# Kernel tuning notes

Hardware: AMD Instinct MI355X
Metric: run time of the kernel (lower is better)

The kernel has to match this reference:

```python
import jax, jax.numpy as jnp
import numpy as np

EMBED = 1024
HEADS = 16
HEAD_DIM = EMBED // HEADS
SCALE = HEAD_DIM ** -0.5


def setup_inputs() -> dict:
    key = jax.random.key(0)
    ks = jax.random.split(key, 9)
    B, N = 2, 2048
    std = EMBED ** -0.5
    return {
        "query": jax.random.normal(ks[0], (B, N, EMBED), jnp.float32),
        "key": jax.random.normal(ks[1], (B, N, EMBED), jnp.float32),
        "value": jax.random.normal(ks[2], (B, N, EMBED), jnp.float32),
        # torch nn.Linear weights are [out, in]; y = x @ W.T + b
        "Wq": jax.random.normal(ks[3], (EMBED, EMBED), jnp.float32) * std,
        "bq": jax.random.normal(ks[4], (EMBED,), jnp.float32) * 0.01,
        "Wk": jax.random.normal(ks[5], (EMBED, EMBED), jnp.float32) * std,
        "bk": jax.random.normal(ks[6], (EMBED,), jnp.float32) * 0.01,
        "Wv": jax.random.normal(ks[7], (EMBED, EMBED), jnp.float32) * std,
        "bv": jax.random.normal(ks[8], (EMBED,), jnp.float32) * 0.01,
    }


def reference(query, key, value, Wq, bq, Wk, bk, Wv, bv):
    B, NQ, _ = query.shape
    NK = key.shape[1]
    q = query @ Wq.T + bq  # [B, NQ, E]
    k = key @ Wk.T + bk    # [B, NK, E]
    v = value @ Wv.T + bv  # [B, NK, E]
    # split heads -> [B, H, N, Dh]
    q = q.reshape(B, NQ, HEADS, HEAD_DIM).transpose(0, 2, 1, 3)
    k = k.reshape(B, NK, HEADS, HEAD_DIM).transpose(0, 2, 1, 3)
    v = v.reshape(B, NK, HEADS, HEAD_DIM).transpose(0, 2, 1, 3)
    attn = jnp.einsum("bhqd,bhkd->bhqk", q, k) * SCALE  # [B, H, NQ, NK]
    attn = jax.nn.softmax(attn, axis=-1)
    out = jnp.einsum("bhqk,bhkd->bhqd", attn, v)  # [B, H, NQ, Dh]
    out = out.transpose(0, 2, 1, 3).reshape(B, NQ, EMBED)
    # o_proj is Identity (odim == embed_dim, o_proj=False); dropout is 0 (eval)
    return out
```

## Files before the change

### kernel.cpp

```cpp
#include <hip/hip_runtime.h>

#define EMB 1024
#define NSEQ 2048
#define NBATCH 2
#define NHEAD 16
#define DHEAD 64
#define QSCALE 0.18033688011112042f

typedef float f32x4 __attribute__((ext_vector_type(4)));
typedef short s16x8 __attribute__((ext_vector_type(8)));
typedef short s16x4 __attribute__((ext_vector_type(4)));

typedef __attribute__((address_space(3))) short lds_short;
typedef __attribute__((address_space(1))) const short glb_short;

__device__ __forceinline__ void gl_lds16(const short* g, short* l) {
    __builtin_amdgcn_global_load_lds((glb_short*)g, (lds_short*)l, 16, 0, 0);
}

__device__ __forceinline__ short bf16r(float f) {
    unsigned u = __float_as_uint(f);
    u += 0x7fffu + ((u >> 16) & 1u);
    return (short)(u >> 16);
}

__device__ __forceinline__ unsigned pkbf(float a, float b) {
#if defined(__has_builtin) && __has_builtin(__builtin_amdgcn_cvt_pk_bf16_f32)
    auto r = __builtin_amdgcn_cvt_pk_bf16_f32(a, b);
    unsigned u;
    __builtin_memcpy(&u, &r, 4);
    return u;
#else
    return ((unsigned)bf16r(a) & 0xffffu) | ((unsigned)bf16r(b) << 16);
#endif
}

__device__ __forceinline__ float fexp2(float x) {
#if defined(__has_builtin) && __has_builtin(__builtin_amdgcn_exp2f)
    return __builtin_amdgcn_exp2f(x);
#else
    return exp2f(x);
#endif
}

__global__ __launch_bounds__(256) void cvt6_kernel(
    const float* __restrict__ s0, const float* __restrict__ s1, const float* __restrict__ s2,
    const float* __restrict__ s3, const float* __restrict__ s4, const float* __restrict__ s5,
    short* __restrict__ d0, short* __restrict__ d1, short* __restrict__ d2,
    short* __restrict__ d3, short* __restrict__ d4, short* __restrict__ d5,
    int n0, int n1, int n2, int n3, int n4, int n5)
{
    const int seg = blockIdx.y;
    const float* s = (seg == 0) ? s0 : (seg == 1) ? s1 : (seg == 2) ? s2
                   : (seg == 3) ? s3 : (seg == 4) ? s4 : s5;
    short* d = (seg == 0) ? d0 : (seg == 1) ? d1 : (seg == 2) ? d2
             : (seg == 3) ? d3 : (seg == 4) ? d4 : d5;
    const int n = (seg == 0) ? n0 : (seg == 1) ? n1 : (seg == 2) ? n2
                : (seg == 3) ? n3 : (seg == 4) ? n4 : n5;

    const int i = (blockIdx.x * 256 + threadIdx.x) * 8;
    if (i >= n) return;
    float4 a = *(const float4*)(s + i);
    float4 b = *(const float4*)(s + i + 4);
    uint4 u = { pkbf(a.x, a.y), pkbf(a.z, a.w), pkbf(b.x, b.y), pkbf(b.z, b.w) };
    *(uint4*)(d + i) = u;
}

__global__ __launch_bounds__(256, 3) void proj2_kernel(
    const short* __restrict__ Xq, const short* __restrict__ Xk, const short* __restrict__ Xv,
    const short* __restrict__ Wq, const short* __restrict__ Wk, const short* __restrict__ Wv,
    const float* __restrict__ bq, const float* __restrict__ bk, const float* __restrict__ bv,
    short* __restrict__ Oq, short* __restrict__ Ok, short* __restrict__ Ov)
{
    const int z = blockIdx.z;
    const short* X    = (z == 0) ? Xq : (z == 1) ? Xk : Xv;
    const short* W    = (z == 0) ? Wq : (z == 1) ? Wk : Wv;
    const float* bias = (z == 0) ? bq : (z == 1) ? bk : bv;
    short* Out        = (z == 0) ? Oq : (z == 1) ? Ok : Ov;
    const float osc   = (z == 0) ? QSCALE : 1.0f;

    const int n0 = blockIdx.x * 128;
    const int m0 = blockIdx.y * 128;

    __shared__ __align__(16) short As[128 * 64];
    __shared__ __align__(16) short Bs[128 * 64];

    const int t    = threadIdx.x;
    const int lane = t & 63;
    const int wave = t >> 6;
    const int r    = lane & 15;
    const int quad = lane >> 4;
    const int wm   = (wave >> 1) * 64;
    const int wn   = (wave & 1) * 64;

    const int p0    = wave * 256 + lane;
    const int row0  = p0 >> 3;
    const int lc0   = (p0 & 7) ^ (row0 & 7);
    const short* gA = X + (size_t)(m0 + row0) * EMB + lc0 * 8;
    const short* gB = W + (size_t)(n0 + row0) * EMB + lc0 * 8;
    short* lA = As + p0 * 8;
    short* lB = Bs + p0 * 8;

    f32x4 acc[4][4];
#pragma unroll
    for (int i = 0; i < 4; ++i)
#pragma unroll
        for (int j = 0; j < 4; ++j)
#pragma unroll
            for (int v = 0; v < 4; ++v) acc[i][j][v] = 0.f;

    for (int k0 = 0; k0 < EMB; k0 += 64) {
#pragma unroll
        for (int i = 0; i < 4; ++i) {
            gl_lds16(gA + k0 + (size_t)8 * i * EMB, lA + i * 512);
            gl_lds16(gB + k0 + (size_t)8 * i * EMB, lB + i * 512);
        }
        __syncthreads();

#pragma unroll
        for (int ks = 0; ks < 2; ++ks) {
            const int fc = ((ks * 4 + quad) ^ (r & 7)) * 8;
            s16x8 af[4], bf[4];
#pragma unroll
            for (int i = 0; i < 4; ++i) af[i] = *(const s16x8*)&As[(wm + i * 16 + r) * 64 + fc];
#pragma unroll
            for (int j = 0; j < 4; ++j) bf[j] = *(const s16x8*)&Bs[(wn + j * 16 + r) * 64 + fc];
#pragma unroll
            for (int i = 0; i < 4; ++i)
#pragma unroll
                for (int j = 0; j < 4; ++j)
                    acc[i][j] = __builtin_amdgcn_mfma_f32_16x16x32_bf16(af[i], bf[j], acc[i][j], 0, 0, 0);
        }
        __syncthreads();
    }

    if (z != 2) {
#pragma unroll
        for (int j = 0; j < 4; ++j) {
            const int gn = n0 + wn + j * 16 + r;
            const float bb = bias[gn];
#pragma unroll
            for (int i = 0; i < 4; ++i)
#pragma unroll
                for (int reg = 0; reg < 4; ++reg) {
                    const int gm = m0 + wm + i * 16 + quad * 4 + reg;
                    Out[(size_t)gm * EMB + gn] = bf16r((acc[i][j][reg] + bb) * osc);
                }
        }
    } else {
#pragma unroll
        for (int j = 0; j < 4; ++j) {
            const int gn = n0 + wn + j * 16 + r;
            const float bb = bias[gn];
            const int hh = gn >> 6;
            const int dd = gn & 63;
#pragma unroll
            for (int i = 0; i < 4; ++i) {
                const int gm = m0 + wm + i * 16 + quad * 4;
                const int bi = gm >> 11;
                const int nn = gm & 2047;
                s16x4 pk;
#pragma unroll
                for (int reg = 0; reg < 4; ++reg) pk[reg] = bf16r(acc[i][j][reg] + bb);
                *(s16x4*)(Out + ((size_t)(bi * NHEAD + hh) * DHEAD + dd) * NSEQ + nn) = pk;
            }
        }
    }
}

__global__ __launch_bounds__(256) void proj_kernel(
    const float* __restrict__ Xq, const float* __restrict__ Xk, const float* __restrict__ Xv,
    const float* __restrict__ Wq, const float* __restrict__ Wk, const float* __restrict__ Wv,
    const float* __restrict__ bq, const float* __restrict__ bk, const float* __restrict__ bv,
    short* __restrict__ Oq, short* __restrict__ Ok, short* __restrict__ Ov)
{
    const int z = blockIdx.z;
    const float* X    = (z == 0) ? Xq : (z == 1) ? Xk : Xv;
    const float* W    = (z == 0) ? Wq : (z == 1) ? Wk : Wv;
    const float* bias = (z == 0) ? bq : (z == 1) ? bk : bv;
    short* Out        = (z == 0) ? Oq : (z == 1) ? Ok : Ov;
    const float osc   = (z == 0) ? QSCALE : 1.0f;

    const int n0 = blockIdx.x * 128;
    const int m0 = blockIdx.y * 128;

    __shared__ __align__(16) short As[128][40];
    __shared__ __align__(16) short Bs[128][40];

    const int t    = threadIdx.x;
    const int lane = t & 63;
    const int wave = t >> 6;
    const int r    = lane & 15;
    const int quad = lane >> 4;
    const int wm   = (wave >> 1) * 64;
    const int wn   = (wave & 1) * 64;

    const int srow = t >> 1;
    const int scol = (t & 1) << 4;

    f32x4 acc[4][4];
#pragma unroll
    for (int i = 0; i < 4; ++i)
#pragma unroll
        for (int j = 0; j < 4; ++j)
#pragma unroll
            for (int v = 0; v < 4; ++v) acc[i][j][v] = 0.f;

    for (int k0 = 0; k0 < EMB; k0 += 32) {
        const float4* xp = (const float4*)(X + (size_t)(m0 + srow) * EMB + k0 + scol);
        const float4* wp = (const float4*)(W + (size_t)(n0 + srow) * EMB + k0 + scol);
        float4 x0 = xp[0], x1 = xp[1], x2 = xp[2], x3 = xp[3];
        float4 w0 = wp[0], w1 = wp[1], w2 = wp[2], w3 = wp[3];
        uint4 a0 = { pkbf(x0.x, x0.y), pkbf(x0.z, x0.w), pkbf(x1.x, x1.y), pkbf(x1.z, x1.w) };
        uint4 a1 = { pkbf(x2.x, x2.y), pkbf(x2.z, x2.w), pkbf(x3.x, x3.y), pkbf(x3.z, x3.w) };
        uint4 b0 = { pkbf(w0.x, w0.y), pkbf(w0.z, w0.w), pkbf(w1.x, w1.y), pkbf(w1.z, w1.w) };
        uint4 b1 = { pkbf(w2.x, w2.y), pkbf(w2.z, w2.w), pkbf(w3.x, w3.y), pkbf(w3.z, w3.w) };
        *(uint4*)&As[srow][scol]     = a0;
        *(uint4*)&As[srow][scol + 8] = a1;
        *(uint4*)&Bs[srow][scol]     = b0;
        *(uint4*)&Bs[srow][scol + 8] = b1;
        __syncthreads();

        s16x8 af[4], bf[4];
#pragma unroll
        for (int i = 0; i < 4; ++i) af[i] = *(const s16x8*)&As[wm + i * 16 + r][quad * 8];
#pragma unroll
        for (int j = 0; j < 4; ++j) bf[j] = *(const s16x8*)&Bs[wn + j * 16 + r][quad * 8];
#pragma unroll
        for (int i = 0; i < 4; ++i)
#pragma unroll
            for (int j = 0; j < 4; ++j)
                acc[i][j] = __builtin_amdgcn_mfma_f32_16x16x32_bf16(af[i], bf[j], acc[i][j], 0, 0, 0);
        __syncthreads();
    }

#pragma unroll
    for (int j = 0; j < 4; ++j) {
        const int gn = n0 + wn + j * 16 + r;
        const float bb = bias[gn];
#pragma unroll
        for (int i = 0; i < 4; ++i)
#pragma unroll
            for (int reg = 0; reg < 4; ++reg) {
                const int gm = m0 + wm + i * 16 + quad * 4 + reg;
                Out[(size_t)gm * EMB + gn] = bf16r((acc[i][j][reg] + bb) * osc);
            }
    }
}

__global__ __launch_bounds__(256) void vtrans_kernel(
    const short* __restrict__ Vp, short* __restrict__ VT)
{
    const int n0 = blockIdx.x * 64;
    const int h  = blockIdx.y;
    const int b  = blockIdx.z;
    __shared__ __align__(16) short L[64][72];

    const int t  = threadIdx.x;
    const int rr = t >> 2;
    const int cc = (t & 3) * 16;

    const short* src = Vp + (size_t)(b * NSEQ + n0 + rr) * EMB + h * DHEAD + cc;
    s16x8 a = *(const s16x8*)src;
    s16x8 c = *(const s16x8*)(src + 8);
    *(s16x8*)&L[rr][cc]     = a;
    *(s16x8*)&L[rr][cc + 8] = c;
    __syncthreads();

    const int d  = t >> 2;
    const int c4 = (t & 3) * 16;
    short vals[16];
#pragma unroll
    for (int i = 0; i < 16; ++i) vals[i] = L[c4 + i][d];
    short* dst = VT + ((size_t)(b * NHEAD + h) * DHEAD + d) * NSEQ + n0 + c4;
    *(s16x8*)dst       = *(s16x8*)&vals[0];
    *(s16x8*)(dst + 8) = *(s16x8*)&vals[8];
}

__global__ __launch_bounds__(256, 2) void attn12_kernel(
    const short* __restrict__ Qp, const short* __restrict__ Kp,
    const short* __restrict__ VT, float* __restrict__ Out)
{
    const int qblk = blockIdx.x * 128;
    const int h    = blockIdx.y;
    const int b    = blockIdx.z;

    __shared__ __align__(16) char smem[65536];
    short* S    = (short*)smem;
    float* fbuf = (float*)smem;

    const int t    = threadIdx.x;
    const int lane = t & 63;
    const int w    = t >> 6;
    const int r    = lane & 15;
    const int quad = lane >> 4;
    const int r7   = r & 7;

    const size_t rowbase = (size_t)b * NSEQ;
    const int    colbase = h * DHEAD;
    const size_t bh64    = (size_t)(b * NHEAD + h) * DHEAD;

    s16x8 qf[2][2];
#pragma unroll
    for (int qs = 0; qs < 2; ++qs)
#pragma unroll
        for (int ks = 0; ks < 2; ++ks)
            qf[qs][ks] = *(const s16x8*)(Qp + (rowbase + qblk + w * 32 + qs * 16 + r) * EMB
                                          + colbase + ks * 32 + quad * 8);

    f32x4 accO[2][4];
#pragma unroll
    for (int qs = 0; qs < 2; ++qs)
#pragma unroll
        for (int dt = 0; dt < 4; ++dt)
#pragma unroll
            for (int v = 0; v < 4; ++v) accO[qs][dt][v] = 0.f;
    float lsum[2] = {0.f, 0.f};
    const f32x4 zf = {0.f, 0.f, 0.f, 0.f};

    const int krow0 = t >> 3;
    const int kgc   = ((t & 7) ^ (krow0 & 7)) * 8;
    const int vrow0 = t >> 4;
    const int vgc   = ((t & 15) ^ (vrow0 & 7)) * 8;
    const short* gKp = Kp + (rowbase + krow0) * EMB + colbase + kgc;
    const short* gVp = VT + (bh64 + vrow0) * NSEQ + vgc;

    {
        short* SK = S;
        short* SV = S + 8192;
#pragma unroll
        for (int i = 0; i < 4; ++i) {
            gl_lds16(gKp + (size_t)i * 32 * EMB, SK + (i * 256 + t) * 8);
            gl_lds16(gVp + (size_t)i * 16 * NSEQ, SV + (i * 256 + t) * 8);
        }
        gKp += (size_t)128 * EMB;
        gVp += 128;
    }
    __syncthreads();

    const int kofs = (quad ^ r7) * 8;
    int vofs[4];
    {
        const int x4  = r7 & 4;
        const int qr3 = ((quad >> 1) ^ r7) & 3;
#pragma unroll
        for (int s = 0; s < 4; ++s)
            vofs[s] = ((((s << 2) ^ x4) | qr3) * 8) + (quad & 1) * 4;
    }

#pragma unroll 2
    for (int it = 0; it < 16; ++it) {
        const int cur = it & 1;

        if (it + 1 < 16) {
            short* SKn = S + (cur ^ 1) * 16384;
            short* SVn = SKn + 8192;
#pragma unroll
            for (int i = 0; i < 4; ++i) {
                gl_lds16(gKp + (size_t)i * 32 * EMB, SKn + (i * 256 + t) * 8);
                gl_lds16(gVp + (size_t)i * 16 * NSEQ, SVn + (i * 256 + t) * 8);
            }
            gKp += (size_t)128 * EMB;
            gVp += 128;
        }

        const short* Ks = S + cur * 16384;
        const short* Vs = Ks + 8192;

        s16x8 pf[2][4];
#pragma unroll
        for (int s = 0; s < 4; ++s) {
            const short* kb = Ks + (s * 32 + r) * 64;
            const s16x8 kf00 = *(const s16x8*)(kb + kofs);
            const s16x8 kf01 = *(const s16x8*)(kb + (kofs ^ 32));
            const s16x8 kf10 = *(const s16x8*)(kb + 1024 + kofs);
            const s16x8 kf11 = *(const s16x8*)(kb + 1024 + (kofs ^ 32));
#pragma unroll
            for (int qs = 0; qs < 2; ++qs) {
                __builtin_amdgcn_s_setprio(1);
                f32x4 s0 = __builtin_amdgcn_mfma_f32_16x16x32_bf16(
                    kf01, qf[qs][1], __builtin_amdgcn_mfma_f32_16x16x32_bf16(kf00, qf[qs][0], zf, 0, 0, 0), 0, 0, 0);
                f32x4 s1 = __builtin_amdgcn_mfma_f32_16x16x32_bf16(
                    kf11, qf[qs][1], __builtin_amdgcn_mfma_f32_16x16x32_bf16(kf10, qf[qs][0], zf, 0, 0, 0), 0, 0, 0);
                __builtin_amdgcn_s_setprio(0);
                float p0[4], p1[4];
#pragma unroll
                for (int reg = 0; reg < 4; ++reg) {
                    p0[reg] = fexp2(s0[reg]);
                    p1[reg] = fexp2(s1[reg]);
                    lsum[qs] += p0[reg] + p1[reg];
                }
                uint4 uu = { pkbf(p0[0], p0[1]), pkbf(p0[2], p0[3]),
                             pkbf(p1[0], p1[1]), pkbf(p1[2], p1[3]) };
                __builtin_memcpy(&pf[qs][s], &uu, 16);
            }
        }

#pragma unroll
        for (int dt = 0; dt < 4; ++dt) {
            const short* vb = Vs + (dt * 16 + r) * 128;
            s16x8 vfl[4];
#pragma unroll
            for (int s = 0; s < 4; ++s) {
                s16x4 lo = *(const s16x4*)(vb + vofs[s]);
                s16x4 hi = *(const s16x4*)(vb + (vofs[s] ^ 16));
                vfl[s] = __builtin_shufflevector(lo, hi, 0, 1, 2, 3, 4, 5, 6, 7);
            }
            __builtin_amdgcn_s_setprio(1);
#pragma unroll
            for (int qs = 0; qs < 2; ++qs)
#pragma unroll
                for (int s = 0; s < 4; ++s)
                    accO[qs][dt] = __builtin_amdgcn_mfma_f32_16x16x32_bf16(vfl[s], pf[qs][s], accO[qs][dt], 0, 0, 0);
            __builtin_amdgcn_s_setprio(0);
        }

        __syncthreads();
    }

    float rl[2];
#pragma unroll
    for (int qs = 0; qs < 2; ++qs) {
        float s = lsum[qs];
        s += __shfl_xor(s, 16);
        s += __shfl_xor(s, 32);
        rl[qs] = 1.f / s;
    }

#pragma unroll
    for (int qs = 0; qs < 2; ++qs) {
        __syncthreads();
#pragma unroll
        for (int dt = 0; dt < 4; ++dt)
#pragma unroll
            for (int reg = 0; reg < 4; ++reg)
                fbuf[(w * 16 + r) * 68 + dt * 16 + quad * 4 + reg] = accO[qs][dt][reg] * rl[qs];
        __syncthreads();
        const int qi   = t >> 2;
        const int c    = (t & 3) * 16;
        const int wsrc = qi >> 4;
        const int rsrc = qi & 15;
        const float4* fp = (const float4*)&fbuf[(wsrc * 16 + rsrc) * 68 + c];
        float4 o0 = fp[0], o1 = fp[1], o2 = fp[2], o3 = fp[3];
        float* op = Out + (rowbase + qblk + wsrc * 32 + qs * 16 + rsrc) * EMB + colbase + c;
        ((float4*)op)[0] = o0;
        ((float4*)op)[1] = o1;
        ((float4*)op)[2] = o2;
        ((float4*)op)[3] = o3;
    }
}

__global__ __launch_bounds__(256) void attn_fb_kernel(
    const short* __restrict__ Qp, const short* __restrict__ Kp,
    const short* __restrict__ Vp, float* __restrict__ Out)
{
    const int qt = blockIdx.x;
    const int h  = blockIdx.y;
    const int b  = blockIdx.z;

    __shared__ __align__(16) short Ks[64][72];
    __shared__ __align__(16) short VsT[64][72];
    __shared__ __align__(16) short Ps[4][16][72];

    const int t    = threadIdx.x;
    const int lane = t & 63;
    const int w    = t >> 6;
    const int r    = lane & 15;
    const int quad = lane >> 4;

    const size_t rowbase = (size_t)b * NSEQ;
    const int colbase    = h * DHEAD;

    const short* Qr = Qp + (rowbase + qt * 64 + w * 16 + r) * EMB + colbase;
    const s16x8 qf0 = *(const s16x8*)(Qr + quad * 8);
    const s16x8 qf1 = *(const s16x8*)(Qr + 32 + quad * 8);

    float mrow[4], lrow[4];
    f32x4 accO[4];
#pragma unroll
    for (int i = 0; i < 4; ++i) {
        mrow[i] = -INFINITY;
        lrow[i] = 0.f;
#pragma unroll
        for (int v = 0; v < 4; ++v) accO[i][v] = 0.f;
    }

    const int srow = t >> 2;
    const int scol = (t & 3) << 4;

    for (int kt = 0; kt < 32; ++kt) {
        const short* Krow = Kp + (rowbase + kt * 64 + srow) * EMB + colbase + scol;
        const short* Vrow = Vp + (rowbase + kt * 64 + srow) * EMB + colbase + scol;
        s16x8 kv0 = *(const s16x8*)Krow;
        s16x8 kv1 = *(const s16x8*)(Krow + 8);
        s16x8 vv0 = *(const s16x8*)Vrow;
        s16x8 vv1 = *(const s16x8*)(Vrow + 8);
        *(s16x8*)&Ks[srow][scol]     = kv0;
        *(s16x8*)&Ks[srow][scol + 8] = kv1;
#pragma unroll
        for (int i = 0; i < 8; ++i) {
            VsT[scol + i][srow]     = vv0[i];
            VsT[scol + 8 + i][srow] = vv1[i];
        }
        __syncthreads();

        f32x4 sacc[4];
#pragma unroll
        for (int j = 0; j < 4; ++j) {
#pragma unroll
            for (int v = 0; v < 4; ++v) sacc[j][v] = 0.f;
            s16x8 kf0 = *(const s16x8*)&Ks[j * 16 + r][quad * 8];
            s16x8 kf1 = *(const s16x8*)&Ks[j * 16 + r][32 + quad * 8];
            sacc[j] = __builtin_amdgcn_mfma_f32_16x16x32_bf16(qf0, kf0, sacc[j], 0, 0, 0);
            sacc[j] = __builtin_amdgcn_mfma_f32_16x16x32_bf16(qf1, kf1, sacc[j], 0, 0, 0);
        }

        float rmax[4];
#pragma unroll
        for (int reg = 0; reg < 4; ++reg) rmax[reg] = -INFINITY;
#pragma unroll
        for (int j = 0; j < 4; ++j)
#pragma unroll
            for (int reg = 0; reg < 4; ++reg)
                rmax[reg] = fmaxf(rmax[reg], sacc[j][reg]);
#pragma unroll
        for (int reg = 0; reg < 4; ++reg) {
#pragma unroll
            for (int mask = 1; mask <= 8; mask <<= 1)
                rmax[reg] = fmaxf(rmax[reg], __shfl_xor(rmax[reg], mask, 64));
        }

        float alpha[4], rsum[4];
#pragma unroll
        for (int reg = 0; reg < 4; ++reg) {
            float mnew = fmaxf(mrow[reg], rmax[reg]);
            alpha[reg] = fexp2(mrow[reg] - mnew);
            mrow[reg]  = mnew;
            rsum[reg]  = 0.f;
        }

#pragma unroll
        for (int j = 0; j < 4; ++j)
#pragma unroll
            for (int reg = 0; reg < 4; ++reg) {
                float p = fexp2(sacc[j][reg] - mrow[reg]);
                rsum[reg] += p;
                Ps[w][quad * 4 + reg][j * 16 + r] = bf16r(p);
            }
#pragma unroll
        for (int reg = 0; reg < 4; ++reg) {
#pragma unroll
            for (int mask = 1; mask <= 8; mask <<= 1)
                rsum[reg] += __shfl_xor(rsum[reg], mask, 64);
            lrow[reg] = lrow[reg] * alpha[reg] + rsum[reg];
        }
#pragma unroll
        for (int j = 0; j < 4; ++j)
#pragma unroll
            for (int reg = 0; reg < 4; ++reg) accO[j][reg] *= alpha[reg];

#pragma unroll
        for (int s = 0; s < 2; ++s) {
            s16x8 pfr = *(const s16x8*)&Ps[w][r][s * 32 + quad * 8];
#pragma unroll
            for (int j = 0; j < 4; ++j) {
                s16x8 vfr = *(const s16x8*)&VsT[j * 16 + r][s * 32 + quad * 8];
                accO[j] = __builtin_amdgcn_mfma_f32_16x16x32_bf16(pfr, vfr, accO[j], 0, 0, 0);
            }
        }
        __syncthreads();
    }

#pragma unroll
    for (int j = 0; j < 4; ++j)
#pragma unroll
        for (int reg = 0; reg < 4; ++reg) {
            const int qrow = qt * 64 + w * 16 + quad * 4 + reg;
            Out[(rowbase + qrow) * EMB + colbase + j * 16 + r] = accO[j][reg] / lrow[reg];
        }
}

extern "C" void kernel_launch(void* const* d_in, const int* in_sizes, int n_in,
                              void* d_out, int out_size, void* d_ws, size_t ws_size,
                              hipStream_t stream) {
    const float* query = (const float*)d_in[0];
    const float* key   = (const float*)d_in[1];
    const float* value = (const float*)d_in[2];
    const float* Wq    = (const float*)d_in[3];
    const float* bq    = (const float*)d_in[4];
    const float* Wk    = (const float*)d_in[5];
    const float* bk    = (const float*)d_in[6];
    const float* Wv    = (const float*)d_in[7];
    const float* bv    = (const float*)d_in[8];
    float* out = (float*)d_out;

    const size_t XBUF = (size_t)NBATCH * NSEQ * EMB;
    const size_t WBUF = (size_t)EMB * EMB;

    short* Qb  = (short*)d_ws;
    short* Kb  = Qb + XBUF;
    short* Vb  = Kb + XBUF;
    short* VTb = Vb + XBUF;
    short* Xqb = VTb + XBUF;
    short* Xkb = Xqb + XBUF;
    short* Xvb = Xkb + XBUF;
    short* Wqb = Xvb + XBUF;
    short* Wkb = Wqb + WBUF;
    short* Wvb = Wkb + WBUF;

    const size_t need_full = (7 * XBUF + 3 * WBUF) * sizeof(short);
    const size_t need_attn = 4 * XBUF * sizeof(short);

    if (ws_size >= need_full) {
        cvt6_kernel<<<dim3(2048, 6), 256, 0, stream>>>(
            query, key, value, Wq, Wk, Wv,
            Xqb, Xkb, Xvb, Wqb, Wkb, Wvb,
            (int)XBUF, (int)XBUF, (int)XBUF, (int)WBUF, (int)WBUF, (int)WBUF);
        proj2_kernel<<<dim3(EMB / 128, (NBATCH * NSEQ) / 128, 3), 256, 0, stream>>>(
            Xqb, Xkb, Xvb, Wqb, Wkb, Wvb, bq, bk, bv, Qb, Kb, VTb);
        attn12_kernel<<<dim3(NSEQ / 128, NHEAD, NBATCH), 256, 0, stream>>>(
            Qb, Kb, VTb, out);
    } else if (ws_size >= need_attn) {
        proj_kernel<<<dim3(EMB / 128, (NBATCH * NSEQ) / 128, 3), 256, 0, stream>>>(
            query, key, value, Wq, Wk, Wv, bq, bk, bv, Qb, Kb, Vb);
        vtrans_kernel<<<dim3(NSEQ / 64, NHEAD, NBATCH), 256, 0, stream>>>(Vb, VTb);
        attn12_kernel<<<dim3(NSEQ / 128, NHEAD, NBATCH), 256, 0, stream>>>(
            Qb, Kb, VTb, out);
    } else {
        proj_kernel<<<dim3(EMB / 128, (NBATCH * NSEQ) / 128, 3), 256, 0, stream>>>(
            query, key, value, Wq, Wk, Wv, bq, bk, bv, Qb, Kb, Vb);
        attn_fb_kernel<<<dim3(NSEQ / 64, NHEAD, NBATCH), 256, 0, stream>>>(Qb, Kb, Vb, out);
    }
}
```

Baseline: 199.6 us.

## Single-buffer attention LDS, compute row sums via MFMA, interleave PV per key slice

```diff
diff --git a/kernel.cpp b/kernel.cpp
--- a/kernel.cpp
+++ b/kernel.cpp
@@ -277,7 +277,7 @@
     *(s16x8*)(dst + 8) = *(s16x8*)&vals[8];
 }
 
-__global__ __launch_bounds__(256, 2) void attn12_kernel(
+__global__ __launch_bounds__(256, 3) void attn13_kernel(
     const short* __restrict__ Qp, const short* __restrict__ Kp,
     const short* __restrict__ VT, float* __restrict__ Out)
 {
@@ -285,8 +285,9 @@
     const int h    = blockIdx.y;
     const int b    = blockIdx.z;
 
-    __shared__ __align__(16) char smem[65536];
-    short* S    = (short*)smem;
+    __shared__ __align__(16) char smem[32768];
+    short* Ks   = (short*)smem;
+    short* Vs   = (short*)smem + 128 * 64;
     float* fbuf = (float*)smem;
 
     const int t    = threadIdx.x;
@@ -309,14 +310,20 @@
                                           + colbase + ks * 32 + quad * 8);
 
     f32x4 accO[2][4];
-#pragma unroll
-    for (int qs = 0; qs < 2; ++qs)
+    f32x4 lacc[2];
+#pragma unroll
+    for (int qs = 0; qs < 2; ++qs) {
+#pragma unroll
+        for (int v = 0; v < 4; ++v) lacc[qs][v] = 0.f;
 #pragma unroll
         for (int dt = 0; dt < 4; ++dt)
 #pragma unroll
             for (int v = 0; v < 4; ++v) accO[qs][dt][v] = 0.f;
-    float lsum[2] = {0.f, 0.f};
+    }
     const f32x4 zf = {0.f, 0.f, 0.f, 0.f};
+    const short one_bf = (short)0x3F80;
+    const s16x8 ones = { one_bf, one_bf, one_bf, one_bf,
+                         one_bf, one_bf, one_bf, one_bf };
 
     const int krow0 = t >> 3;
     const int kgc   = ((t & 7) ^ (krow0 & 7)) * 8;
@@ -325,19 +332,6 @@
     const short* gKp = Kp + (rowbase + krow0) * EMB + colbase + kgc;
     const short* gVp = VT + (bh64 + vrow0) * NSEQ + vgc;
 
-    {
-        short* SK = S;
-        short* SV = S + 8192;
-#pragma unroll
-        for (int i = 0; i < 4; ++i) {
-            gl_lds16(gKp + (size_t)i * 32 * EMB, SK + (i * 256 + t) * 8);
-            gl_lds16(gVp + (size_t)i * 16 * NSEQ, SV + (i * 256 + t) * 8);
-        }
-        gKp += (size_t)128 * EMB;
-        gVp += 128;
-    }
-    __syncthreads();
-
     const int kofs = (quad ^ r7) * 8;
     int vofs[4];
     {
@@ -348,26 +342,16 @@
             vofs[s] = ((((s << 2) ^ x4) | qr3) * 8) + (quad & 1) * 4;
     }
 
-#pragma unroll 2
     for (int it = 0; it < 16; ++it) {
-        const int cur = it & 1;
-
-        if (it + 1 < 16) {
-            short* SKn = S + (cur ^ 1) * 16384;
-            short* SVn = SKn + 8192;
-#pragma unroll
-            for (int i = 0; i < 4; ++i) {
-                gl_lds16(gKp + (size_t)i * 32 * EMB, SKn + (i * 256 + t) * 8);
-                gl_lds16(gVp + (size_t)i * 16 * NSEQ, SVn + (i * 256 + t) * 8);
-            }
-            gKp += (size_t)128 * EMB;
-            gVp += 128;
-        }
-
-        const short* Ks = S + cur * 16384;
-        const short* Vs = Ks + 8192;
-
-        s16x8 pf[2][4];
+#pragma unroll
+        for (int i = 0; i < 4; ++i) {
+            gl_lds16(gKp + (size_t)i * 32 * EMB, Ks + (i * 256 + t) * 8);
+            gl_lds16(gVp + (size_t)i * 16 * NSEQ, Vs + (i * 256 + t) * 8);
+        }
+        gKp += (size_t)128 * EMB;
+        gVp += 128;
+        __syncthreads();
+
 #pragma unroll
         for (int s = 0; s < 4; ++s) {
             const short* kb = Ks + (s * 32 + r) * 64;
@@ -375,6 +359,7 @@
             const s16x8 kf01 = *(const s16x8*)(kb + (kofs ^ 32));
             const s16x8 kf10 = *(const s16x8*)(kb + 1024 + kofs);
             const s16x8 kf11 = *(const s16x8*)(kb + 1024 + (kofs ^ 32));
+            s16x8 pf_s[2];
 #pragma unroll
             for (int qs = 0; qs < 2; ++qs) {
                 __builtin_amdgcn_s_setprio(1);
@@ -383,49 +368,32 @@
                 f32x4 s1 = __builtin_amdgcn_mfma_f32_16x16x32_bf16(
                     kf11, qf[qs][1], __builtin_amdgcn_mfma_f32_16x16x32_bf16(kf10, qf[qs][0], zf, 0, 0, 0), 0, 0, 0);
                 __builtin_amdgcn_s_setprio(0);
-                float p0[4], p1[4];
-#pragma unroll
-                for (int reg = 0; reg < 4; ++reg) {
-                    p0[reg] = fexp2(s0[reg]);
-                    p1[reg] = fexp2(s1[reg]);
-                    lsum[qs] += p0[reg] + p1[reg];
-                }
-                uint4 uu = { pkbf(p0[0], p0[1]), pkbf(p0[2], p0[3]),
-                             pkbf(p1[0], p1[1]), pkbf(p1[2], p1[3]) };
-                __builtin_memcpy(&pf[qs][s], &uu, 16);
+                const float e0 = fexp2(s0[0]), e1 = fexp2(s0[1]);
+                const float e2 = fexp2(s0[2]), e3 = fexp2(s0[3]);
+                const float e4 = fexp2(s1[0]), e5 = fexp2(s1[1]);
+                const float e6 = fexp2(s1[2]), e7 = fexp2(s1[3]);
+                uint4 uu = { pkbf(e0, e1), pkbf(e2, e3), pkbf(e4, e5), pkbf(e6, e7) };
+                __builtin_memcpy(&pf_s[qs], &uu, 16);
+                lacc[qs] = __builtin_amdgcn_mfma_f32_16x16x32_bf16(ones, pf_s[qs], lacc[qs], 0, 0, 0);
             }
-        }
-
-#pragma unroll
-        for (int dt = 0; dt < 4; ++dt) {
-            const short* vb = Vs + (dt * 16 + r) * 128;
-            s16x8 vfl[4];
-#pragma unroll
-            for (int s = 0; s < 4; ++s) {
+#pragma unroll
+            for (int dt = 0; dt < 4; ++dt) {
+                const short* vb = Vs + (dt * 16 + r) * 128;
                 s16x4 lo = *(const s16x4*)(vb + vofs[s]);
                 s16x4 hi = *(const s16x4*)(vb + (vofs[s] ^ 16));
-                vfl[s] = __builtin_shufflevector(lo, hi, 0, 1, 2, 3, 4, 5, 6, 7);
+                s16x8 vfl = __builtin_shufflevector(lo, hi, 0, 1, 2, 3, 4, 5, 6, 7);
+                __builtin_amdgcn_s_setprio(1);
+                accO[0][dt] = __builtin_amdgcn_mfma_f32_16x16x32_bf16(vfl, pf_s[0], accO[0][dt], 0, 0, 0);
+                accO[1][dt] = __builtin_amdgcn_mfma_f32_16x16x32_bf16(vfl, pf_s[1], accO[1][dt], 0, 0, 0);
+                __builtin_amdgcn_s_setprio(0);
             }
-            __builtin_amdgcn_s_setprio(1);
-#pragma unroll
-            for (int qs = 0; qs < 2; ++qs)
-#pragma unroll
-                for (int s = 0; s < 4; ++s)
-                    accO[qs][dt] = __builtin_amdgcn_mfma_f32_16x16x32_bf16(vfl[s], pf[qs][s], accO[qs][dt], 0, 0, 0);
-            __builtin_amdgcn_s_setprio(0);
-        }
-
+        }
         __syncthreads();
     }
 
     float rl[2];
 #pragma unroll
-    for (int qs = 0; qs < 2; ++qs) {
-        float s = lsum[qs];
-        s += __shfl_xor(s, 16);
-        s += __shfl_xor(s, 32);
-        rl[qs] = 1.f / s;
-    }
+    for (int qs = 0; qs < 2; ++qs) rl[qs] = 1.f / lacc[qs][0];
 
 #pragma unroll
     for (int qs = 0; qs < 2; ++qs) {
@@ -618,13 +586,13 @@
             (int)XBUF, (int)XBUF, (int)XBUF, (int)WBUF, (int)WBUF, (int)WBUF);
         proj2_kernel<<<dim3(EMB / 128, (NBATCH * NSEQ) / 128, 3), 256, 0, stream>>>(
             Xqb, Xkb, Xvb, Wqb, Wkb, Wvb, bq, bk, bv, Qb, Kb, VTb);
-        attn12_kernel<<<dim3(NSEQ / 128, NHEAD, NBATCH), 256, 0, stream>>>(
+        attn13_kernel<<<dim3(NSEQ / 128, NHEAD, NBATCH), 256, 0, stream>>>(
             Qb, Kb, VTb, out);
     } else if (ws_size >= need_attn) {
         proj_kernel<<<dim3(EMB / 128, (NBATCH * NSEQ) / 128, 3), 256, 0, stream>>>(
             query, key, value, Wq, Wk, Wv, bq, bk, bv, Qb, Kb, Vb);
         vtrans_kernel<<<dim3(NSEQ / 64, NHEAD, NBATCH), 256, 0, stream>>>(Vb, VTb);
-        attn12_kernel<<<dim3(NSEQ / 128, NHEAD, NBATCH), 256, 0, stream>>>(
+        attn13_kernel<<<dim3(NSEQ / 128, NHEAD, NBATCH), 256, 0, stream>>>(
             Qb, Kb, VTb, out);
     } else {
         proj_kernel<<<dim3(EMB / 128, (NBATCH * NSEQ) / 128, 3), 256, 0, stream>>>(
```

After: 202.8 us (median of 3 runs). No clear change (+1.6%).
